# Kernel optimization log

Measured on AMD Instinct MI355X. Metric: run time of the kernel, lower is better.

## Reference

```python
import jax, jax.numpy as jnp
import numpy as np

EPS = 1e-12

def _agnn(x, src, dst, beta, n):
    # L2-normalize node features (F.normalize semantics: clamp norm at eps)
    norm = jnp.maximum(jnp.linalg.norm(x, axis=-1, keepdims=True), EPS)
    xn = x / norm
    # cosine similarity per edge, scaled by learnable beta
    a = beta * jnp.sum(xn[dst] * xn[src], axis=-1)  # [E]
    # numerically-stable softmax over incoming edges of each target node
    amax = jax.ops.segment_max(a, dst, num_segments=n)            # [N]
    e = jnp.exp(a - amax[dst])                                     # [E]
    denom = jax.ops.segment_sum(e, dst, num_segments=n)           # [N]
    alpha = e / jnp.maximum(denom[dst], EPS)                       # [E]
    # weighted scatter-add aggregation of source features
    return jax.ops.segment_sum(alpha[:, None] * x[src], dst, num_segments=n)


def setup_inputs() -> dict:
    key = jax.random.key(0)
    ks = jax.random.split(key, 6)
    N, E, F_in, C = 50000, 800000, 1024, 256
    x = jax.random.normal(ks[0], (N, F_in), dtype=jnp.float32)
    edge_index = jax.random.randint(ks[1], (2, E), 0, N, dtype=jnp.int64)
    lin1_w = jax.random.normal(ks[2], (64, F_in), dtype=jnp.float32) / np.sqrt(F_in)
    lin1_b = jax.random.normal(ks[3], (64,), dtype=jnp.float32) * 0.01
    beta1 = jnp.ones((1,), dtype=jnp.float32)
    beta2 = jnp.ones((1,), dtype=jnp.float32)
    lin2_w = jax.random.normal(ks[4], (C, 64), dtype=jnp.float32) / np.sqrt(64.0)
    lin2_b = jax.random.normal(ks[5], (C,), dtype=jnp.float32) * 0.01
    return {"x": x, "edge_index": edge_index, "lin1_w": lin1_w, "lin1_b": lin1_b,
            "beta1": beta1, "beta2": beta2, "lin2_w": lin2_w, "lin2_b": lin2_b}


def reference(x, edge_index, lin1_w, lin1_b, beta1, beta2, lin2_w, lin2_b):
    n = x.shape[0]
    src, dst = edge_index[0], edge_index[1]  # PyG: row0 = source j, row1 = target i
    # dropout is identity in eval mode
    h = jax.nn.relu(jnp.einsum('nf,hf->nh', x, lin1_w) + lin1_b)  # [N, 64]
    h = _agnn(h, src, dst, beta1[0], n)
    h = _agnn(h, src, dst, beta2[0], n)
    logits = jnp.einsum('nh,ch->nc', h, lin2_w) + lin2_b          # [N, C]
    return jax.nn.log_softmax(logits, axis=1)
```

## Files before the change

kernel.cpp:

```cpp
#include <hip/hip_runtime.h>
#include <hip/hip_bf16.h>

#define EPSF 1e-12f
#define CAP 128

typedef __attribute__((ext_vector_type(8))) short short8;
typedef __attribute__((ext_vector_type(4))) float f32x4;

__device__ __forceinline__ short f2bf(float f) {
    union { float f; unsigned u; } v; v.f = f;
    unsigned r = v.u + 0x7fffu + ((v.u >> 16) & 1u);
    return (short)(r >> 16);
}
__device__ __forceinline__ float bf2f(ushort u) {
    return __uint_as_float((unsigned)u << 16);
}
__device__ __forceinline__ void gload_lds16(const void* g, void* l) {
    __builtin_amdgcn_global_load_lds(
        (const __attribute__((address_space(1))) void*)g,
        (__attribute__((address_space(3))) void*)l, 16, 0, 0);
}

__global__ __launch_bounds__(256) void prep_kernel(const float4* __restrict__ W1,
                                                   const float4* __restrict__ W2,
                                                   ushort* __restrict__ W1b,
                                                   ushort* __restrict__ W2b,
                                                   int* __restrict__ cnt, int N) {
    int i = blockIdx.x * 256 + threadIdx.x;
    const float4* Wp; ushort* Wo; int idx;
    if (i < 16384) { Wp = W1; Wo = W1b; idx = i; }
    else           { Wp = W2; Wo = W2b; idx = i - 16384; }
    float4 v = Wp[idx];
    ushort4 o;
    o.x = (ushort)f2bf(v.x); o.y = (ushort)f2bf(v.y);
    o.z = (ushort)f2bf(v.z); o.w = (ushort)f2bf(v.w);
    *(ushort4*)(Wo + 4 * (size_t)idx) = o;
    int n4 = N >> 2;
    if (i < n4) ((int4*)cnt)[i] = make_int4(0, 0, 0, 0);
}

__global__ __launch_bounds__(256) void lin1_scatter_kernel(const float* __restrict__ x,
                                                           const ushort* __restrict__ Wb,
                                                           const float* __restrict__ b,
                                                           ushort* __restrict__ xnb,
                                                           float* __restrict__ nrm_out,
                                                           const int* __restrict__ src,
                                                           const int* __restrict__ dst,
                                                           int* __restrict__ cnt,
                                                           int* __restrict__ esrcb,
                                                           int nLin1, int N, int E) {
    __shared__ float sxf[4][16][256];

    if ((int)blockIdx.x >= nLin1) {
        int e = ((int)blockIdx.x - nLin1) * 256 + threadIdx.x;
        if (e < E) {
            int d = dst[e];
            int p = atomicAdd(&cnt[d], 1);
            if (p < CAP) esrcb[(d << 7) + p] = src[e];
        }
        return;
    }

    const int lane = threadIdx.x & 63;
    const int wv = threadIdx.x >> 6;
    const int rbase = blockIdx.x * 16;
    const int r15 = lane & 15;
    const int kg = lane >> 4;

    {
        const char* xq = (const char*)(x + (size_t)rbase * 1024 + wv * 256);
        int colb = lane * 16;
#pragma unroll
        for (int r = 0; r < 16; ++r) {
            gload_lds16(xq + (size_t)r * 4096 + (colb ^ ((r & 7) << 5)),
                        &sxf[wv][r][0]);
        }
        asm volatile("s_waitcnt vmcnt(0)" ::: "memory");
        __builtin_amdgcn_sched_barrier(0);
    }

    f32x4 acc[4];
#pragma unroll
    for (int t = 0; t < 4; ++t) acc[t] = (f32x4){0.f, 0.f, 0.f, 0.f};

    const ushort* wp0 = Wb + (size_t)r15 * 1024 + wv * 256 + kg * 8;
    const char* arow = (const char*)&sxf[wv][r15][0];
    const int rsw = (r15 & 7) << 5;

#pragma unroll
    for (int k0 = 0; k0 < 256; k0 += 32) {
        const float4* p = (const float4*)(arow + (((kg * 8 + k0) * 4) ^ rsw));
        float4 f0 = p[0];
        float4 f1 = p[1];
        short8 af;
        af[0] = f2bf(f0.x); af[1] = f2bf(f0.y); af[2] = f2bf(f0.z); af[3] = f2bf(f0.w);
        af[4] = f2bf(f1.x); af[5] = f2bf(f1.y); af[6] = f2bf(f1.z); af[7] = f2bf(f1.w);
#pragma unroll
        for (int t = 0; t < 4; ++t) {
            short8 bf_ = *(const short8*)(wp0 + (size_t)t * 16 * 1024 + k0);
            acc[t] = __builtin_amdgcn_mfma_f32_16x16x32_bf16(af, bf_, acc[t], 0, 0, 0);
        }
    }

    float (*red)[16][68] = (float(*)[16][68])sxf;
    __syncthreads();
#pragma unroll
    for (int t = 0; t < 4; ++t)
#pragma unroll
        for (int r = 0; r < 4; ++r)
            red[wv][kg * 4 + r][t * 16 + r15] = acc[t][r];
    __syncthreads();

    const int tid = threadIdx.x;
#pragma unroll
    for (int q = 0; q < 4; ++q) {
        int idx = q * 256 + tid;
        int nloc = idx >> 6, c = idx & 63;
        float v = red[0][nloc][c] + red[1][nloc][c] + red[2][nloc][c] + red[3][nloc][c];
        float hv = fmaxf(v + b[c], 0.f);
        float ss = hv * hv;
#pragma unroll
        for (int off = 32; off; off >>= 1) ss += __shfl_xor(ss, off);
        float nrm = fmaxf(sqrtf(ss), EPSF);
        int node = rbase + nloc;
        if (node < N) {
            xnb[(size_t)node * 64 + c] = (ushort)f2bf(hv / nrm);
            if (c == 0) nrm_out[node] = nrm;
        }
    }
}

__global__ __launch_bounds__(256) void agnn_fused_kernel(const ushort* __restrict__ xnb,
                                                         const float* __restrict__ nrm,
                                                         const int* __restrict__ cnt,
                                                         const int* __restrict__ esrcb,
                                                         const float* __restrict__ beta,
                                                         ushort* __restrict__ xnb_out,
                                                         float* __restrict__ nrm_out, int N) {
    const int lane = threadIdx.x & 63;
    const int l = lane & 15;
    int node = (blockIdx.x * 256 + threadIdx.x) >> 4;
    bool valid = node < N;
    int nodec = valid ? node : N - 1;

    int deg = cnt[nodec]; if (deg > CAP) deg = CAP;
    const int* eb = esrcb + (nodec << 7);
    ushort4 xd4 = *(const ushort4*)(xnb + (size_t)nodec * 64 + 4 * l);
    float xd0 = bf2f(xd4.x), xd1 = bf2f(xd4.y), xd2 = bf2f(xd4.z), xd3 = bf2f(xd4.w);
    float bet = beta[0];

    float sum = 0.f;
    float4 acc = make_float4(0.f, 0.f, 0.f, 0.f);

    int k = 0;
    for (; k + 3 < deg; k += 4) {
        int s0i = eb[k], s1i = eb[k + 1], s2i = eb[k + 2], s3i = eb[k + 3];
        ushort4 v0 = *(const ushort4*)(xnb + (size_t)s0i * 64 + 4 * l);
        ushort4 v1 = *(const ushort4*)(xnb + (size_t)s1i * 64 + 4 * l);
        ushort4 v2 = *(const ushort4*)(xnb + (size_t)s2i * 64 + 4 * l);
        ushort4 v3 = *(const ushort4*)(xnb + (size_t)s3i * 64 + 4 * l);
        float n0 = nrm[s0i], n1 = nrm[s1i], n2 = nrm[s2i], n3 = nrm[s3i];
        float a0 = bf2f(v0.x), a1 = bf2f(v0.y), a2 = bf2f(v0.z), a3 = bf2f(v0.w);
        float b0 = bf2f(v1.x), b1 = bf2f(v1.y), b2 = bf2f(v1.z), b3 = bf2f(v1.w);
        float c0 = bf2f(v2.x), c1 = bf2f(v2.y), c2 = bf2f(v2.z), c3 = bf2f(v2.w);
        float d0 = bf2f(v3.x), d1 = bf2f(v3.y), d2 = bf2f(v3.z), d3 = bf2f(v3.w);
        float pa = a0 * xd0 + a1 * xd1 + a2 * xd2 + a3 * xd3;
        float pb = b0 * xd0 + b1 * xd1 + b2 * xd2 + b3 * xd3;
        float pc = c0 * xd0 + c1 * xd1 + c2 * xd2 + c3 * xd3;
        float pd = d0 * xd0 + d1 * xd1 + d2 * xd2 + d3 * xd3;
        pa += __shfl_xor(pa, 1); pb += __shfl_xor(pb, 1);
        pc += __shfl_xor(pc, 1); pd += __shfl_xor(pd, 1);
        pa += __shfl_xor(pa, 2); pb += __shfl_xor(pb, 2);
        pc += __shfl_xor(pc, 2); pd += __shfl_xor(pd, 2);
        pa += __shfl_xor(pa, 4); pb += __shfl_xor(pb, 4);
        pc += __shfl_xor(pc, 4); pd += __shfl_xor(pd, 4);
        pa += __shfl_xor(pa, 8); pb += __shfl_xor(pb, 8);
        pc += __shfl_xor(pc, 8); pd += __shfl_xor(pd, 8);
        float wa = __expf(bet * pa), wb = __expf(bet * pb);
        float wc = __expf(bet * pc), wd = __expf(bet * pd);
        float wna = wa * n0, wnb = wb * n1, wnc = wc * n2, wnd = wd * n3;
        sum += (wa + wb) + (wc + wd);
        acc.x += wna * a0 + wnb * b0 + wnc * c0 + wnd * d0;
        acc.y += wna * a1 + wnb * b1 + wnc * c1 + wnd * d1;
        acc.z += wna * a2 + wnb * b2 + wnc * c2 + wnd * d2;
        acc.w += wna * a3 + wnb * b3 + wnc * c3 + wnd * d3;
    }
    for (; k < deg; ++k) {
        int sa = eb[k];
        ushort4 va = *(const ushort4*)(xnb + (size_t)sa * 64 + 4 * l);
        float na = nrm[sa];
        float a0 = bf2f(va.x), a1 = bf2f(va.y), a2 = bf2f(va.z), a3 = bf2f(va.w);
        float pa = a0 * xd0 + a1 * xd1 + a2 * xd2 + a3 * xd3;
        pa += __shfl_xor(pa, 1); pa += __shfl_xor(pa, 2);
        pa += __shfl_xor(pa, 4); pa += __shfl_xor(pa, 8);
        float wa = __expf(bet * pa);
        float wna = wa * na;
        sum += wa;
        acc.x += wna * a0; acc.y += wna * a1;
        acc.z += wna * a2; acc.w += wna * a3;
    }

    float r = 1.f / fmaxf(sum, EPSF);
    float ox = acc.x * r, oy = acc.y * r, oz = acc.z * r, ow = acc.w * r;
    if (valid) {
        if (nrm_out) {
            float ss = ox * ox + oy * oy + oz * oz + ow * ow;
            ss += __shfl_xor(ss, 1); ss += __shfl_xor(ss, 2);
            ss += __shfl_xor(ss, 4); ss += __shfl_xor(ss, 8);
            float nr = fmaxf(sqrtf(ss), EPSF);
            float ri = 1.f / nr;
            ushort4 ob;
            ob.x = (ushort)f2bf(ox * ri); ob.y = (ushort)f2bf(oy * ri);
            ob.z = (ushort)f2bf(oz * ri); ob.w = (ushort)f2bf(ow * ri);
            *(ushort4*)(xnb_out + (size_t)node * 64 + 4 * l) = ob;
            if (l == 0) nrm_out[node] = nr;
        } else {
            ushort4 ob;
            ob.x = (ushort)f2bf(ox); ob.y = (ushort)f2bf(oy);
            ob.z = (ushort)f2bf(oz); ob.w = (ushort)f2bf(ow);
            *(ushort4*)(xnb_out + (size_t)node * 64 + 4 * l) = ob;
        }
    }
}

__global__ __launch_bounds__(256) void lin2_mfma_ls_kernel(const ushort* __restrict__ h2b,
                                                           const ushort* __restrict__ W2b,
                                                           const float* __restrict__ b,
                                                           float* __restrict__ out, int N) {
    const int lane = threadIdx.x & 63;
    const int wv = threadIdx.x >> 6;
    const int nbase = blockIdx.x * 64 + wv * 16;
    const int r15 = lane & 15;
    const int kg = lane >> 4;

    int an = nbase + r15; if (an >= N) an = N - 1;
    const ushort* ap = h2b + (size_t)an * 64 + kg * 8;
    short8 a0 = *(const short8*)(ap);
    short8 a1 = *(const short8*)(ap + 32);

    f32x4 acc[16];
#pragma unroll
    for (int t = 0; t < 16; ++t) {
        const ushort* wp = W2b + (size_t)(t * 16 + r15) * 64 + kg * 8;
        short8 b0 = *(const short8*)(wp);
        short8 b1 = *(const short8*)(wp + 32);
        acc[t] = __builtin_amdgcn_mfma_f32_16x16x32_bf16(a0, b0, (f32x4){0.f,0.f,0.f,0.f}, 0, 0, 0);
        acc[t] = __builtin_amdgcn_mfma_f32_16x16x32_bf16(a1, b1, acc[t], 0, 0, 0);
    }

#pragma unroll
    for (int t = 0; t < 16; ++t) {
        float bc = b[t * 16 + r15];
        acc[t][0] += bc; acc[t][1] += bc; acc[t][2] += bc; acc[t][3] += bc;
    }

#pragma unroll
    for (int r = 0; r < 4; ++r) {
        float mx = -1e30f;
#pragma unroll
        for (int t = 0; t < 16; ++t) mx = fmaxf(mx, acc[t][r]);
        mx = fmaxf(mx, __shfl_xor(mx, 1)); mx = fmaxf(mx, __shfl_xor(mx, 2));
        mx = fmaxf(mx, __shfl_xor(mx, 4)); mx = fmaxf(mx, __shfl_xor(mx, 8));
        float s = 0.f;
#pragma unroll
        for (int t = 0; t < 16; ++t) s += __expf(acc[t][r] - mx);
        s += __shfl_xor(s, 1); s += __shfl_xor(s, 2);
        s += __shfl_xor(s, 4); s += __shfl_xor(s, 8);
        float lse = mx + __logf(s);
        int node = nbase + kg * 4 + r;
        if (node < N) {
            float* op = out + (size_t)node * 256 + r15;
#pragma unroll
            for (int t = 0; t < 16; ++t) op[t * 16] = acc[t][r] - lse;
        }
    }
}

extern "C" void kernel_launch(void* const* d_in, const int* in_sizes, int n_in,
                              void* d_out, int out_size, void* d_ws, size_t ws_size,
                              hipStream_t stream) {
    const float* x      = (const float*)d_in[0];
    const int*   ei     = (const int*)d_in[1];
    const float* W1     = (const float*)d_in[2];
    const float* b1     = (const float*)d_in[3];
    const float* beta1  = (const float*)d_in[4];
    const float* beta2  = (const float*)d_in[5];
    const float* W2     = (const float*)d_in[6];
    const float* b2     = (const float*)d_in[7];
    float* out = (float*)d_out;

    const int N = in_sizes[0] / 1024;
    const int E = in_sizes[1] / 2;
    const int* src = ei;
    const int* dst = ei + E;

    char* ws = (char*)d_ws;
    const size_t XB = (size_t)N * 64 * sizeof(ushort);
    ushort* xn0b = (ushort*)(ws);
    ushort* xn1b = (ushort*)(ws + XB);
    ushort* h2b  = (ushort*)(ws + 2 * XB);
    size_t off = 3 * XB;
    float* norm0  = (float*)(ws + off); off += (size_t)N * sizeof(float);
    float* norm1  = (float*)(ws + off); off += (size_t)N * sizeof(float);
    int*   cnt    = (int*)(ws + off);   off += (size_t)N * sizeof(int);
    off = (off + 255) & ~(size_t)255;
    int*   esrcb  = (int*)(ws + off);   off += (size_t)N * CAP * sizeof(int);
    ushort* W1b   = (ushort*)(ws + off); off += 64 * 1024 * sizeof(ushort);
    ushort* W2b   = (ushort*)(ws + off); off += 256 * 64 * sizeof(ushort);

    const int gLin1 = (N + 15) / 16;
    const int gE    = (E + 255) / 256;
    const int gNode = (N + 15) / 16;
    const int gLin2 = (N + 63) / 64;

    prep_kernel<<<80, 256, 0, stream>>>((const float4*)W1, (const float4*)W2,
                                        W1b, W2b, cnt, N);
    lin1_scatter_kernel<<<gLin1 + gE, 256, 0, stream>>>(x, W1b, b1, xn0b, norm0,
                                                        src, dst, cnt, esrcb,
                                                        gLin1, N, E);

    agnn_fused_kernel<<<gNode, 256, 0, stream>>>(xn0b, norm0, cnt, esrcb, beta1,
                                                 xn1b, norm1, N);
    agnn_fused_kernel<<<gNode, 256, 0, stream>>>(xn1b, norm1, cnt, esrcb, beta2,
                                                 h2b, nullptr, N);

    lin2_mfma_ls_kernel<<<gLin2, 256, 0, stream>>>(h2b, W2b, b2, out, N);
}
```

Baseline: 198.1 us.

## Interleave lin1 and edge-scatter blocks, stage x as bf16 in LDS via registers

Lin1 blocks and edge-scatter blocks are now interleaved by block parity instead of running as two contiguous ranges, so the atomic-heavy scatter work overlaps the bandwidth-bound GEMM. The x tile is loaded into registers, converted to bf16 once and stored swizzled to LDS, replacing the direct global-to-LDS fp32 copy and the repeated per-k conversion. LDS use drops from 64KB to 32KB, which may allow more resident blocks. In exchange, 16 float4 registers are held per thread, and the padded grid launches idle blocks that exit immediately.

```diff
diff --git a/kernel.cpp b/kernel.cpp
--- a/kernel.cpp
+++ b/kernel.cpp
@@ -14,11 +14,6 @@
 }
 __device__ __forceinline__ float bf2f(ushort u) {
     return __uint_as_float((unsigned)u << 16);
-}
-__device__ __forceinline__ void gload_lds16(const void* g, void* l) {
-    __builtin_amdgcn_global_load_lds(
-        (const __attribute__((address_space(1))) void*)g,
-        (__attribute__((address_space(3))) void*)l, 16, 0, 0);
 }
 
 __global__ __launch_bounds__(256) void prep_kernel(const float4* __restrict__ W1,
@@ -49,10 +44,13 @@
                                                            int* __restrict__ cnt,
                                                            int* __restrict__ esrcb,
                                                            int nLin1, int N, int E) {
-    __shared__ float sxf[4][16][256];
-
-    if ((int)blockIdx.x >= nLin1) {
-        int e = ((int)blockIdx.x - nLin1) * 256 + threadIdx.x;
+    __shared__ ushort sx[16384];
+    const int bid = (int)blockIdx.x;
+    const int role = bid & 1;
+    const int sub = bid >> 1;
+
+    if (role == 1) {
+        int e = sub * 256 + threadIdx.x;
         if (e < E) {
             int d = dst[e];
             int p = atomicAdd(&cnt[d], 1);
@@ -60,23 +58,27 @@
         }
         return;
     }
+    if (sub >= nLin1) return;
 
     const int lane = threadIdx.x & 63;
     const int wv = threadIdx.x >> 6;
-    const int rbase = blockIdx.x * 16;
+    const int rbase = sub * 16;
     const int r15 = lane & 15;
     const int kg = lane >> 4;
 
-    {
-        const char* xq = (const char*)(x + (size_t)rbase * 1024 + wv * 256);
-        int colb = lane * 16;
-#pragma unroll
-        for (int r = 0; r < 16; ++r) {
-            gload_lds16(xq + (size_t)r * 4096 + (colb ^ ((r & 7) << 5)),
-                        &sxf[wv][r][0]);
-        }
-        asm volatile("s_waitcnt vmcnt(0)" ::: "memory");
-        __builtin_amdgcn_sched_barrier(0);
+    float4 xa[16];
+#pragma unroll
+    for (int r = 0; r < 16; ++r) {
+        int row = rbase + r; if (row >= N) row = N - 1;
+        xa[r] = *(const float4*)(x + (size_t)row * 1024 + wv * 256 + lane * 4);
+    }
+    ushort* myq = sx + wv * 4096;
+#pragma unroll
+    for (int r = 0; r < 16; ++r) {
+        ushort4 o;
+        o.x = (ushort)f2bf(xa[r].x); o.y = (ushort)f2bf(xa[r].y);
+        o.z = (ushort)f2bf(xa[r].z); o.w = (ushort)f2bf(xa[r].w);
+        *(ushort4*)(myq + r * 256 + ((lane * 4) ^ ((r & 7) << 3))) = o;
     }
 
     f32x4 acc[4];
@@ -84,17 +86,12 @@
     for (int t = 0; t < 4; ++t) acc[t] = (f32x4){0.f, 0.f, 0.f, 0.f};
 
     const ushort* wp0 = Wb + (size_t)r15 * 1024 + wv * 256 + kg * 8;
-    const char* arow = (const char*)&sxf[wv][r15][0];
-    const int rsw = (r15 & 7) << 5;
+    const ushort* arow_lds = myq + r15 * 256;
+    const int rsw = (r15 & 7) << 3;
 
 #pragma unroll
     for (int k0 = 0; k0 < 256; k0 += 32) {
-        const float4* p = (const float4*)(arow + (((kg * 8 + k0) * 4) ^ rsw));
-        float4 f0 = p[0];
-        float4 f1 = p[1];
-        short8 af;
-        af[0] = f2bf(f0.x); af[1] = f2bf(f0.y); af[2] = f2bf(f0.z); af[3] = f2bf(f0.w);
-        af[4] = f2bf(f1.x); af[5] = f2bf(f1.y); af[6] = f2bf(f1.z); af[7] = f2bf(f1.w);
+        short8 af = *(const short8*)(arow_lds + (((kg * 8) + k0) ^ rsw));
 #pragma unroll
         for (int t = 0; t < 4; ++t) {
             short8 bf_ = *(const short8*)(wp0 + (size_t)t * 16 * 1024 + k0);
@@ -102,7 +99,7 @@
         }
     }
 
-    float (*red)[16][68] = (float(*)[16][68])sxf;
+    float (*red)[16][68] = (float(*)[16][68])sx;
     __syncthreads();
 #pragma unroll
     for (int t = 0; t < 4; ++t)
@@ -310,14 +307,15 @@
 
     const int gLin1 = (N + 15) / 16;
     const int gE    = (E + 255) / 256;
+    const int gFused = 2 * ((gLin1 > gE) ? gLin1 : gE);
     const int gNode = (N + 15) / 16;
     const int gLin2 = (N + 63) / 64;
 
     prep_kernel<<<80, 256, 0, stream>>>((const float4*)W1, (const float4*)W2,
                                         W1b, W2b, cnt, N);
-    lin1_scatter_kernel<<<gLin1 + gE, 256, 0, stream>>>(x, W1b, b1, xn0b, norm0,
-                                                        src, dst, cnt, esrcb,
-                                                        gLin1, N, E);
+    lin1_scatter_kernel<<<gFused, 256, 0, stream>>>(x, W1b, b1, xn0b, norm0,
+                                                    src, dst, cnt, esrcb,
+                                                    gLin1, N, E);
 
     agnn_fused_kernel<<<gNode, 256, 0, stream>>>(xn0b, norm0, cnt, esrcb, beta1,
                                                  xn1b, norm1, N);
```

Measured after the change: 234.5 us. 1.18x slower.

## Give each wave its own rows in lin1 and double-buffer K chunks

Applied to the files above, without the earlier changes.

The lin1 GEMM previously split K across the four waves of a block and summed partials through LDS with block barriers. Now each wave owns 16 rows and walks the full K=1024 in 16 chunks. Global-to-LDS loads are double-buffered so the next chunk loads while the current one feeds the MFMAs. The cross-wave reduction and __syncthreads are gone, and normalization runs straight from the accumulator registers. The cost is a smaller LDS footprint but four times fewer lin1 blocks, plus more waitcnt stalls per wave.

```diff
diff --git a/kernel.cpp b/kernel.cpp
--- a/kernel.cpp
+++ b/kernel.cpp
@@ -49,10 +49,11 @@
                                                            int* __restrict__ cnt,
                                                            int* __restrict__ esrcb,
                                                            int nLin1, int N, int E) {
-    __shared__ float sxf[4][16][256];
-
-    if ((int)blockIdx.x >= nLin1) {
-        int e = ((int)blockIdx.x - nLin1) * 256 + threadIdx.x;
+    __shared__ char slds[4][2][4096];
+    const int bid = (int)blockIdx.x;
+
+    if (bid >= nLin1) {
+        int e = (bid - nLin1) * 256 + threadIdx.x;
         if (e < E) {
             int d = dst[e];
             int p = atomicAdd(&cnt[d], 1);
@@ -63,69 +64,86 @@
 
     const int lane = threadIdx.x & 63;
     const int wv = threadIdx.x >> 6;
-    const int rbase = blockIdx.x * 16;
+    const int rbase = bid * 64 + wv * 16;
     const int r15 = lane & 15;
     const int kg = lane >> 4;
-
-    {
-        const char* xq = (const char*)(x + (size_t)rbase * 1024 + wv * 256);
-        int colb = lane * 16;
-#pragma unroll
-        for (int r = 0; r < 16; ++r) {
-            gload_lds16(xq + (size_t)r * 4096 + (colb ^ ((r & 7) << 5)),
-                        &sxf[wv][r][0]);
-        }
-        asm volatile("s_waitcnt vmcnt(0)" ::: "memory");
+    const int rsw = (r15 & 7) << 5;
+
+    const char* xb = (const char*)x;
+    const int irow4 = lane >> 4;
+    const int icl = lane & 15;
+
+#define ISSUE_CHUNK(c, buf)                                                         \
+    {                                                                               \
+        _Pragma("unroll")                                                           \
+        for (int j = 0; j < 4; ++j) {                                               \
+            int rl = 4 * j + irow4;                                                 \
+            int rg = rbase + rl; if (rg >= N) rg = N - 1;                           \
+            gload_lds16(xb + (size_t)rg * 4096 + (c) * 256 +                        \
+                            ((icl * 16) ^ ((rl & 7) << 5)),                         \
+                        &slds[wv][buf][j * 1024]);                                  \
+        }                                                                           \
+    }
+
+    f32x4 acc[4];
+#pragma unroll
+    for (int t = 0; t < 4; ++t) acc[t] = (f32x4){0.f, 0.f, 0.f, 0.f};
+
+    ISSUE_CHUNK(0, 0)
+    ISSUE_CHUNK(1, 1)
+
+#pragma unroll
+    for (int c = 0; c < 16; ++c) {
+        if (c < 15) { asm volatile("s_waitcnt vmcnt(4)" ::: "memory"); }
+        else        { asm volatile("s_waitcnt vmcnt(0)" ::: "memory"); }
         __builtin_amdgcn_sched_barrier(0);
-    }
-
-    f32x4 acc[4];
-#pragma unroll
-    for (int t = 0; t < 4; ++t) acc[t] = (f32x4){0.f, 0.f, 0.f, 0.f};
-
-    const ushort* wp0 = Wb + (size_t)r15 * 1024 + wv * 256 + kg * 8;
-    const char* arow = (const char*)&sxf[wv][r15][0];
-    const int rsw = (r15 & 7) << 5;
-
-#pragma unroll
-    for (int k0 = 0; k0 < 256; k0 += 32) {
-        const float4* p = (const float4*)(arow + (((kg * 8 + k0) * 4) ^ rsw));
-        float4 f0 = p[0];
-        float4 f1 = p[1];
-        short8 af;
-        af[0] = f2bf(f0.x); af[1] = f2bf(f0.y); af[2] = f2bf(f0.z); af[3] = f2bf(f0.w);
-        af[4] = f2bf(f1.x); af[5] = f2bf(f1.y); af[6] = f2bf(f1.z); af[7] = f2bf(f1.w);
+
+        const char* arow = &slds[wv][c & 1][0] + r15 * 256;
+#pragma unroll
+        for (int kl = 0; kl < 2; ++kl) {
+            int lc = (kg * 32 + kl * 128) ^ rsw;
+            float4 f0 = *(const float4*)(arow + lc);
+            float4 f1 = *(const float4*)(arow + lc + 16);
+            short8 af;
+            af[0] = f2bf(f0.x); af[1] = f2bf(f0.y); af[2] = f2bf(f0.z); af[3] = f2bf(f0.w);
+            af[4] = f2bf(f1.x); af[5] = f2bf(f1.y); af[6] = f2bf(f1.z); af[7] = f2bf(f1.w);
+            int kstep = c * 2 + kl;
+#pragma unroll
+            for (int t = 0; t < 4; ++t) {
+                short8 bf_ = *(const short8*)(Wb + (size_t)(t * 16 + r15) * 1024 +
+                                              kstep * 32 + kg * 8);
+                acc[t] = __builtin_amdgcn_mfma_f32_16x16x32_bf16(af, bf_, acc[t], 0, 0, 0);
+            }
+        }
+        asm volatile("s_waitcnt lgkmcnt(0)" ::: "memory");
+        __builtin_amdgcn_sched_barrier(0);
+        if (c + 2 < 16) ISSUE_CHUNK(c + 2, c & 1)
+    }
+#undef ISSUE_CHUNK
+
+    float bb[4];
+#pragma unroll
+    for (int t = 0; t < 4; ++t) bb[t] = b[t * 16 + r15];
+
+#pragma unroll
+    for (int reg = 0; reg < 4; ++reg) {
+        float hv[4];
+        float ss = 0.f;
 #pragma unroll
         for (int t = 0; t < 4; ++t) {
-            short8 bf_ = *(const short8*)(wp0 + (size_t)t * 16 * 1024 + k0);
-            acc[t] = __builtin_amdgcn_mfma_f32_16x16x32_bf16(af, bf_, acc[t], 0, 0, 0);
-        }
-    }
-
-    float (*red)[16][68] = (float(*)[16][68])sxf;
-    __syncthreads();
-#pragma unroll
-    for (int t = 0; t < 4; ++t)
-#pragma unroll
-        for (int r = 0; r < 4; ++r)
-            red[wv][kg * 4 + r][t * 16 + r15] = acc[t][r];
-    __syncthreads();
-
-    const int tid = threadIdx.x;
-#pragma unroll
-    for (int q = 0; q < 4; ++q) {
-        int idx = q * 256 + tid;
-        int nloc = idx >> 6, c = idx & 63;
-        float v = red[0][nloc][c] + red[1][nloc][c] + red[2][nloc][c] + red[3][nloc][c];
-        float hv = fmaxf(v + b[c], 0.f);
-        float ss = hv * hv;
-#pragma unroll
-        for (int off = 32; off; off >>= 1) ss += __shfl_xor(ss, off);
+            hv[t] = fmaxf(acc[t][reg] + bb[t], 0.f);
+            ss += hv[t] * hv[t];
+        }
+        ss += __shfl_xor(ss, 1); ss += __shfl_xor(ss, 2);
+        ss += __shfl_xor(ss, 4); ss += __shfl_xor(ss, 8);
         float nrm = fmaxf(sqrtf(ss), EPSF);
-        int node = rbase + nloc;
+        int node = rbase + kg * 4 + reg;
         if (node < N) {
-            xnb[(size_t)node * 64 + c] = (ushort)f2bf(hv / nrm);
-            if (c == 0) nrm_out[node] = nrm;
+            float ri = 1.f / nrm;
+#pragma unroll
+            for (int t = 0; t < 4; ++t)
+                xnb[(size_t)node * 64 + t * 16 + r15] = (ushort)f2bf(hv[t] * ri);
+            if (r15 == 0) nrm_out[node] = nrm;
         }
     }
 }
@@ -308,7 +326,7 @@
     ushort* W1b   = (ushort*)(ws + off); off += 64 * 1024 * sizeof(ushort);
     ushort* W2b   = (ushort*)(ws + off); off += 256 * 64 * sizeof(ushort);
 
-    const int gLin1 = (N + 15) / 16;
+    const int gLin1 = (N + 63) / 64;
     const int gE    = (E + 255) / 256;
     const int gNode = (N + 15) / 16;
     const int gLin2 = (N + 63) / 64;
```

After: 194.0 us. -2.1%, faster.
